# Kernel optimization log

Measured on AMD Instinct MI355X. Metric: run time of the kernel, lower is better.

## Reference

```python
import jax, jax.numpy as jnp
import numpy as np


def _gru_dir(x, Wih, Whh, bih, bhh):
    # x: (B,T,I) -> (B,T,H); torch GRU equations, h0 = 0
    H = Whh.shape[1]
    pre = x @ Wih.T + bih  # (B,T,3H), input projection hoisted out of scan
    def step(h, p):
        gh = h @ Whh.T + bhh
        pr, pz, pn = jnp.split(p, 3, axis=-1)
        gr, gz, gn = jnp.split(gh, 3, axis=-1)
        r = jax.nn.sigmoid(pr + gr)
        z = jax.nn.sigmoid(pz + gz)
        n = jnp.tanh(pn + r * gn)
        h = (1.0 - z) * n + z * h
        return h, h
    h0 = jnp.zeros((x.shape[0], H), x.dtype)
    _, ys = jax.lax.scan(step, h0, jnp.swapaxes(pre, 0, 1))
    return jnp.swapaxes(ys, 0, 1)


def _gru_bidir(x, Wih, Whh, bih, bhh):
    f = _gru_dir(x, Wih[0], Whh[0], bih[0], bhh[0])
    b = _gru_dir(x[:, ::-1], Wih[1], Whh[1], bih[1], bhh[1])[:, ::-1]
    return jnp.concatenate([f, b], axis=-1)


def _forward(inputs, embed, l_Wih, l_Whh, l_bih, l_bhh, r_Wih, r_Whh, r_bih, r_bhh,
             a_Wih, a_Whh, a_bih, a_bhh, Wc1, Wc2, vc, Wb, Wd, vd, Wm, vm, Ws, vs,
             Wp, vp, Wpred):
    x = embed[inputs]  # (B,T,E)
    hl = _gru_bidir(x, l_Wih, l_Whh, l_bih, l_bhh)  # (B,T,2H)
    hr = _gru_bidir(x, r_Wih, r_Whh, r_bih, r_bhh)  # (B,T,2H)
    # co-attention: score[b,i,j] = vc . tanh(Wc1 hl_j + Wc2 hr_i)
    s = jnp.tanh((hl @ Wc1.T)[:, None, :, :] + (hr @ Wc2.T)[:, :, None, :])  # (B,T,T,H)
    ptc = jax.nn.softmax((s @ vc.T)[..., 0], axis=-1) @ hl
    # bilinear: hr (Wb hl)^T
    sjt = jnp.einsum('bid,bjd->bij', hr, hl @ Wb.T)
    ptb = jax.nn.softmax(sjt, axis=-1) @ hl
    # multiplicative: vd . tanh(Wd (hl_j * hr_i))
    p = hl[:, None, :, :] * hr[:, :, None, :]  # (B,T,T,2H)
    ptd = jax.nn.softmax((jnp.tanh(p @ Wd.T) @ vd.T)[..., 0], axis=-1) @ hl
    # subtractive: vm . tanh(Wm (hl_j - hr_i))
    d = hl[:, None, :, :] - hr[:, :, None, :]  # (B,T,T,2H)
    ptm = jax.nn.softmax((jnp.tanh(d @ Wm.T) @ vm.T)[..., 0], axis=-1) @ hl
    # self-attention on hr: vs . tanh(Ws (hr_j * hr_i))
    ss = hr[:, None, :, :] * hr[:, :, None, :]  # (B,T,T,2H)
    pts = jax.nn.softmax((jnp.tanh(ss @ Ws.T) @ vs.T)[..., 0], axis=-1) @ hr
    agg = jnp.concatenate([hr, pts, ptc, ptd, ptb, ptm], axis=-1)  # (B,T,12H)
    ar = _gru_bidir(agg, a_Wih, a_Whh, a_bih, a_bhh)  # (B,T,2H)
    # pooling of hl
    sj = jax.nn.softmax(jnp.swapaxes(jnp.tanh(hl @ Wp.T) @ vp.T, 1, 2), axis=-1)  # (B,1,T)
    rl = sj @ hl  # (B,1,2H)
    # final attention over aggregation
    sj2 = jax.nn.softmax(jnp.swapaxes((ar @ Wc1.T + rl @ Wc2.T) @ vc.T, 1, 2), axis=-1)  # (B,1,T)
    rr = (sj2 @ ar)[:, 0, :]  # (B,2H)
    return jax.nn.sigmoid(rr @ Wpred.T)  # (B,labels)


def setup_inputs() -> dict:
    B, T, V, E, H, L = 4, 256, 30000, 300, 128, 2
    key = jax.random.key(0)
    ks = jax.random.split(key, 40)
    inp = {}
    inp['inputs'] = jax.random.randint(ks[0], (B, T), 0, V)
    inp['embed'] = jax.random.uniform(ks[1], (V, E), jnp.float32, -0.1, 0.1)
    ki = 2
    for name, isz in [('l', E), ('r', E), ('a', 12 * H)]:
        inp[name + '_Wih'] = jax.random.normal(ks[ki], (2, 3 * H, isz), jnp.float32) * 0.05; ki += 1
        inp[name + '_Whh'] = jax.random.normal(ks[ki], (2, 3 * H, H), jnp.float32) * 0.05; ki += 1
        inp[name + '_bih'] = jnp.zeros((2, 3 * H), jnp.float32)
        inp[name + '_bhh'] = jnp.zeros((2, 3 * H), jnp.float32)
    for n, o, i in [('Wc1', H, 2 * H), ('Wc2', H, 2 * H), ('vc', 1, H), ('Wb', 2 * H, 2 * H),
                    ('Wd', H, 2 * H), ('vd', 1, H), ('Wm', H, 2 * H), ('vm', 1, H),
                    ('Ws', H, 2 * H), ('vs', 1, H), ('Wp', H, 2 * H), ('vp', 1, H),
                    ('Wpred', L, 2 * H)]:
        inp[n] = jax.random.normal(ks[ki], (o, i), jnp.float32) * 0.05; ki += 1
    return inp


def reference(inputs, embed, l_Wih, l_Whh, l_bih, l_bhh, r_Wih, r_Whh, r_bih, r_bhh,
              a_Wih, a_Whh, a_bih, a_bhh, Wc1, Wc2, vc, Wb, Wd, vd, Wm, vm, Ws, vs,
              Wp, vp, Wpred):
    return _forward(inputs, embed, l_Wih, l_Whh, l_bih, l_bhh, r_Wih, r_Whh, r_bih,
                    r_bhh, a_Wih, a_Whh, a_bih, a_bhh, Wc1, Wc2, vc, Wb, Wd, vd, Wm,
                    vm, Ws, vs, Wp, vp, Wpred)
```

## Files before the change

### kernel.cpp

```cpp
#include <hip/hip_runtime.h>


#define DEV static __device__ __forceinline__
#define BAR_LGKM() __asm__ volatile("s_waitcnt lgkmcnt(0)\ns_barrier" ::: "memory")

typedef __attribute__((ext_vector_type(4))) float f32x4;
typedef __attribute__((ext_vector_type(8))) short s16x8;
typedef __attribute__((ext_vector_type(4))) unsigned int u32x4;
typedef __attribute__((ext_vector_type(2))) unsigned int u32x2;

constexpr int T = 256, E = 300, EP = 320, H = 128, H2 = 256, H3 = 384, H12 = 1536;
constexpr int M = 1024;
constexpr int STY = 262144;

DEV float b2f(unsigned short h) { return __uint_as_float(((unsigned)h) << 16); }
DEV unsigned short f2b(float f) {
  unsigned u = __float_as_uint(f);
  u += 0x7fff + ((u >> 16) & 1);
  return (unsigned short)(u >> 16);
}
DEV unsigned cvt_pk_bf16(float lo, float hi) {
  unsigned r;
  __asm__("v_cvt_pk_bf16_f32 %0, %1, %2" : "=v"(r) : "v"(lo), "v"(hi));
  return r;
}
DEV float rcp_f(float x) {
  float r;
  __asm__("v_rcp_f32 %0, %1" : "=v"(r) : "v"(x));
  return r;
}
DEV float sigm(float x) { return rcp_f(1.f + __expf(-x)); }
DEV float tanh_f(float x) {
  float e = __expf(2.f * x);
  return __builtin_fmaf(-2.f, rcp_f(e + 1.f), 1.f);
}
DEV float plsel(float x0, float x1) {
  u32x2 r = __builtin_amdgcn_permlane32_swap(
      __float_as_uint(x0), __float_as_uint(x1), false, false);
  return __uint_as_float(r[0]);
}

DEV s16x8 ldfrag(const unsigned short* p) {
  u32x4 v = *(const u32x4*)p;
  return __builtin_bit_cast(s16x8, v);
}
DEV f32x4 mfma16(s16x8 a, s16x8 b, f32x4 c) {
  return __builtin_amdgcn_mfma_f32_16x16x32_bf16(a, b, c, 0, 0, 0);
}


struct StageArgs {
  const float* cs[9]; unsigned short* cd[9]; int cn[9];
  const int* idx; const float* emb; unsigned short* xhi; unsigned short* xlo;
  const float* lW; const float* rW; unsigned short* wpad;
  int bo[12];
};

__global__ void k_stage(StageArgs sa) {
  int blk = blockIdx.x;
  int seg = 0;
  #pragma unroll
  for (int s2 = 1; s2 < 11; ++s2) seg = (blk >= sa.bo[s2]) ? s2 : seg;
  int i = (blk - sa.bo[seg]) * 256 + threadIdx.x;
  if (seg < 9) {
    if (i < sa.cn[seg]) sa.cd[seg][i] = f2b(sa.cs[seg][i]);
    return;
  }
  if (seg == 9) {
    if (i >= M * EP) return;
    int m = i / EP, e = i - m * EP;
    int r = sa.idx[m];
    float v = (e < E) ? sa.emb[(size_t)r * E + e] : 0.f;
    unsigned short hi = f2b(v);
    sa.xhi[i] = hi;
    sa.xlo[i] = f2b(v - b2f(hi));
    return;
  }
  if (i >= 4 * H3 * EP) return;
  int e = i % EP, n = (i / EP) % H3, uu = i / (EP * H3);
  const float* src = (uu < 2 ? sa.lW : sa.rW) + (size_t)((uu & 1) * H3 + n) * E;
  sa.wpad[i] = (e < E) ? f2b(src[e]) : (unsigned short)0;
}


struct GemmDesc {
  const unsigned short* Ahi; const unsigned short* Alo; const unsigned short* W;
  const float* bias; float* Cf; int N; int K; int tr;
};
struct GemmBatch { GemmDesc d[8]; };

DEV void gemm_body(const GemmDesc& g, int mb, int nb, int tid) {
  int lane = tid & 63, w = tid >> 6, quad = lane >> 4, l16 = lane & 15;
  int K = g.K;
  const unsigned short* Ahp = g.Ahi + (size_t)(mb + w * 16 + l16) * K + quad * 8;
  const unsigned short* Alp = g.Alo + (size_t)(mb + w * 16 + l16) * K + quad * 8;
  const unsigned short* Wp = g.W + (size_t)(nb + l16) * K + quad * 8;
  f32x4 acc[4];
  #pragma unroll
  for (int nt = 0; nt < 4; ++nt) acc[nt] = f32x4{0.f, 0.f, 0.f, 0.f};
  for (int k = 0; k < K; k += 32) {
    s16x8 ah = ldfrag(Ahp + k);
    s16x8 al = ldfrag(Alp + k);
    #pragma unroll
    for (int nt = 0; nt < 4; ++nt) {
      s16x8 b = ldfrag(Wp + (size_t)nt * 16 * K + k);
      acc[nt] = mfma16(ah, b, acc[nt]);
      acc[nt] = mfma16(al, b, acc[nt]);
    }
  }
  int mr0 = mb + w * 16 + quad * 4;
  #pragma unroll
  for (int nt = 0; nt < 4; ++nt) {
    int col = nb + nt * 16 + l16;
    float bv = g.bias ? g.bias[col] : 0.f;
    #pragma unroll
    for (int r = 0; r < 4; ++r) {
      if (g.tr)
        g.Cf[(size_t)col * M + (mr0 + r)] = acc[nt][r] + bv;
      else
        g.Cf[(size_t)(mr0 + r) * g.N + col] = acc[nt][r] + bv;
    }
  }
}

__global__ __launch_bounds__(256) void k_gemm(GemmBatch gb) {
  GemmDesc g = gb.d[blockIdx.z];
  int nb = blockIdx.y * 64;
  if (nb >= g.N) return;
  gemm_body(g, blockIdx.x * 64, nb, threadIdx.x);
}


struct RecArgs {
  const unsigned short* whh[4];
  const float* pre[4];
  float* outf[4];
  unsigned short* outhi[4];
  unsigned short* outlo[4];
  unsigned short* agghi[4];
  unsigned short* agglo[4];
  const float* bhh[4];
  int colOff[4];
  int dir[4];
};

#define GRU_STEP(pr_, pz_, pn_, pq_, hcur_, hnxt_)                             \
  {                                                                            \
    float pr = pr_, pz = pz_, pn = pn_;                                        \
    pq_ += pst2;                                                               \
    pr_ = pq_[0] + bh_r; pz_ = pq_[128] + bh_z; pn_ = pq_[256];                \
    const unsigned short* hb_ = hcur_ + l16 * 136 + quad * 8;                  \
    s16x8 ah0 = ldfrag(hb_);                                                   \
    s16x8 ah1 = ldfrag(hb_ + 32);                                              \
    s16x8 ah2 = ldfrag(hb_ + 64);                                              \
    s16x8 ah3 = ldfrag(hb_ + 96);                                              \
    f32x4 z4 = f32x4{0.f, 0.f, 0.f, 0.f};                                      \
    f32x4 aR0 = mfma16(ah0, bq[0][0], z4);                                     \
    f32x4 aR1 = mfma16(ah2, bq[0][2], z4);                                     \
    aR0 = mfma16(ah1, bq[0][1], aR0);                                          \
    aR1 = mfma16(ah3, bq[0][3], aR1);                                          \
    f32x4 aZ0 = mfma16(ah0, bq[1][0], z4);                                     \
    f32x4 aZ1 = mfma16(ah2, bq[1][2], z4);                                     \
    aZ0 = mfma16(ah1, bq[1][1], aZ0);                                          \
    aZ1 = mfma16(ah3, bq[1][3], aZ1);                                          \
    float r0 = (aR0[0] + aR1[0]) + (aR0[1] + aR1[1]);                          \
    float r1v = (aR0[2] + aR1[2]) + (aR0[3] + aR1[3]);                         \
    float rg = sigm(pr + plsel(r0, r1v));                                      \
    f32x4 aN0 = mfma16(ah0, bq[2][0], z4);                                     \
    f32x4 aN1 = mfma16(ah2, bq[2][2], z4);                                     \
    aN0 = mfma16(ah1, bq[2][1], aN0);                                          \
    aN1 = mfma16(ah3, bq[2][3], aN1);                                          \
    float z0 = (aZ0[0] + aZ1[0]) + (aZ0[1] + aZ1[1]);                          \
    float z1 = (aZ0[2] + aZ1[2]) + (aZ0[3] + aZ1[3]);                          \
    float zg = sigm(pz + plsel(z0, z1));                                       \
    float n0 = (aN0[0] + aN1[0]) + (aN0[1] + aN1[1]);                          \
    float n1 = (aN0[2] + aN1[2]) + (aN0[3] + aN1[3]);                          \
    float ng = tanh_f(pn + rg * (plsel(n0, n1) + bh_n));                       \
    hf = __builtin_fmaf(zg, hf - ng, ng);                                      \
    unsigned hp32 = cvt_pk_bf16(hf, hf);                                       \
    float rem = hf - __uint_as_float(hp32 << 16);                              \
    unsigned lp32 = cvt_pk_bf16(rem, rem);                                     \
    unsigned short hi = (unsigned short)hp32;                                  \
    unsigned short lo = (unsigned short)lp32;                                  \
    hnxt_[(2 * b) * 136 + d] = hi;                                             \
    hnxt_[(2 * b + 1) * 136 + d] = lo;                                         \
    *outf_p = hf; *outhi_p = hi; *outlo_p = lo;                                \
    outf_p += ost; outhi_p += ost; outlo_p += ost;                             \
    if (agghi_p) { *agghi_p = hi; *agglo_p = lo; agghi_p += ast; agglo_p += ast; } \
    BAR_LGKM();                                                                \
  }

__global__ __launch_bounds__(512) void k_gru(RecArgs ra) {
  int u = blockIdx.x;
  __shared__ __align__(16) unsigned short hs[2][16 * 136];
  int tid = threadIdx.x, lane = tid & 63, w8 = tid >> 6;
  int quad = lane >> 4, l16 = lane & 15;
  for (int i = tid; i < 2 * 16 * 136; i += 512) ((unsigned short*)hs)[i] = 0;
  const unsigned short* whh = ra.whh[u];
  s16x8 bq[3][4];
  #pragma unroll
  for (int g = 0; g < 3; ++g) {
    int row = g * 128 + w8 * 16 + l16;
    #pragma unroll
    for (int kc = 0; kc < 4; ++kc)
      bq[g][kc] = ldfrag(whh + (size_t)row * H + kc * 32 + quad * 8);
  }
  const float* bhh = ra.bhh[u];
  const float* pre = ra.pre[u];
  int colOff = ra.colOff[u], dir = ra.dir[u];
  int b = ((quad & 1) << 1) | (quad >> 1);
  int d = w8 * 16 + l16;
  float bh_r = bhh[d], bh_z = bhh[d + 128], bh_n = bhh[d + 256];
  float hf = 0.f;
  int t0 = dir ? (T - 1) : 0;
  long pst = dir ? -(long)H3 : (long)H3;
  long pst2 = 2 * pst;
  long ost = dir ? -(long)H2 : (long)H2;
  long ast = dir ? -(long)H12 : (long)H12;
  size_t o0 = (size_t)(b * T + t0) * H2 + colOff + d;
  size_t a0 = (size_t)(b * T + t0) * H12 + colOff + d;
  float* outf_p = ra.outf[u] + o0;
  unsigned short* outhi_p = ra.outhi[u] + o0;
  unsigned short* outlo_p = ra.outlo[u] + o0;
  unsigned short* agghi_p = ra.agghi[u] ? ra.agghi[u] + a0 : nullptr;
  unsigned short* agglo_p = ra.agglo[u] ? ra.agglo[u] + a0 : nullptr;
  const float* pqE = pre + (size_t)(b * T + t0) * H3 + d;
  const float* pqO = pqE + pst;
  float e_pr = pqE[0] + bh_r, e_pz = pqE[128] + bh_z, e_pn = pqE[256];
  float o_pr = pqO[0] + bh_r, o_pz = pqO[128] + bh_z, o_pn = pqO[256];
  __syncthreads();
  for (int s = 0; s < T; s += 2) {
    GRU_STEP(e_pr, e_pz, e_pn, pqE, hs[0], hs[1]);
    GRU_STEP(o_pr, o_pz, o_pn, pqO, hs[1], hs[0]);
  }
}


struct ScMMArgs {
  const unsigned short* Xhi[2];
  const float* Rf; const float* Wt[2]; const float* vt[2];
  float* So[2]; float* So2[2];
};
struct FuseArgs { GemmDesc d[6]; ScMMArgs sm; };

__global__ __launch_bounds__(256, 2) void k_fuse(FuseArgs fa) {
  __shared__ __align__(16) unsigned short w_lds[64 * 256];
  int y = blockIdx.y;
  int tid = threadIdx.x;
  if (y < 6) {
    int xx = blockIdx.x;
    if (xx >= 64) return;
    GemmDesc g = fa.d[y];
    int nb = (xx >> 4) * 64;
    if (nb >= g.N) return;
    gemm_body(g, (xx & 15) * 64, nb, tid);
    return;
  }
  const ScMMArgs& a = fa.sm;
  int which = y - 6;
  int bi = blockIdx.x, b = bi >> 8;
  int type = which >> 1, khb = which & 1;
  const unsigned short* Xhi = a.Xhi[type];
  const float* W = a.Wt[type] + (size_t)khb * 64 * 256;
  const float* v = a.vt[type] + khb * 64;
  float* Sout = khb ? a.So2[type] : a.So[type];
  int lane = tid & 63, w = tid >> 6, quad = lane >> 4, l16 = lane & 15;
  int d4 = tid & 63, rhi = tid >> 6;
  float4 h4 = ((const float4*)(a.Rf + (size_t)bi * 256))[d4];
  #pragma unroll
  for (int it = 0; it < 16; ++it) {
    int kl = it * 4 + rhi;
    float4 w4 = ((const float4*)(W + (size_t)kl * 256))[d4];
    unsigned lo32 = cvt_pk_bf16(w4.x * h4.x, w4.y * h4.y);
    unsigned hi32 = cvt_pk_bf16(w4.z * h4.z, w4.w * h4.w);
    unsigned long long pk = (unsigned long long)lo32 | ((unsigned long long)hi32 << 32);
    int gphys = ((d4 >> 1) + kl) & 31;
    *(unsigned long long*)(w_lds + (size_t)kl * 256 + gphys * 8 + (d4 & 1) * 4) = pk;
  }
  BAR_LGKM();
  f32x4 acc[4][4];
  #pragma unroll
  for (int jj = 0; jj < 4; ++jj)
    #pragma unroll
    for (int c = 0; c < 4; ++c) acc[jj][c] = f32x4{0.f, 0.f, 0.f, 0.f};
  const unsigned short* Xp0 =
      Xhi + (size_t)(b * 256 + w * 4 * 16 + l16) * 256 + quad * 8;
  #pragma unroll 2
  for (int kc = 0; kc < 8; ++kc) {
    s16x8 af[4];
    #pragma unroll
    for (int c = 0; c < 4; ++c) {
      int krow = c * 16 + l16;
      int gp = (kc * 4 + quad + krow) & 31;
      af[c] = ldfrag(w_lds + (size_t)krow * 256 + gp * 8);
    }
    s16x8 bf[4];
    #pragma unroll
    for (int jj = 0; jj < 4; ++jj)
      bf[jj] = ldfrag(Xp0 + (size_t)jj * 16 * 256 + kc * 32);
    #pragma unroll
    for (int jj = 0; jj < 4; ++jj)
      #pragma unroll
      for (int c = 0; c < 4; ++c)
        acc[jj][c] = mfma16(af[c], bf[jj], acc[jj][c]);
  }
  float vv[4][4];
  #pragma unroll
  for (int c = 0; c < 4; ++c)
    #pragma unroll
    for (int r = 0; r < 4; ++r) vv[c][r] = v[c * 16 + quad * 4 + r];
  #pragma unroll
  for (int jj = 0; jj < 4; ++jj) {
    float s = 0.f;
    #pragma unroll
    for (int c = 0; c < 4; ++c)
      #pragma unroll
      for (int r = 0; r < 4; ++r) s += tanh_f(acc[jj][c][r]) * vv[c][r];
    s += __shfl_xor(s, 16);
    s += __shfl_xor(s, 32);
    int jt = w * 4 + jj;
    if (lane < 16) Sout[(size_t)bi * 256 + jt * 16 + l16] = s;
  }
}


struct ScCmbArgs {
  const float *Hc, *Rc, *Hm, *Rm, *HB, *hrf, *vcf, *vmf; float* S;
};

__global__ __launch_bounds__(256, 2) void k_sccmb(ScCmbArgs a) {
  int bi = blockIdx.x;
  int tid = threadIdx.x;
  __shared__ float rc_l[4 * 128];
  __shared__ float rm_l[4 * 128];
  __shared__ float hr_l[4 * 256];
  __shared__ float vc_l[128], vm_l[128];
  int b = bi >> 6, i0 = (bi & 63) << 2;
  int gi0 = b * 256 + i0;
  {
    const float4* hr4 = (const float4*)(a.hrf + (size_t)gi0 * 256);
    ((float4*)hr_l)[tid] = hr4[tid];
    if (tid < 128) {
      const float4* rc4 = (const float4*)(a.Rc + (size_t)gi0 * 128);
      const float4* rm4 = (const float4*)(a.Rm + (size_t)gi0 * 128);
      ((float4*)rc_l)[tid] = rc4[tid];
      ((float4*)rm_l)[tid] = rm4[tid];
      vc_l[tid] = a.vcf[tid]; vm_l[tid] = a.vmf[tid];
    }
  }
  __syncthreads();
  int j = tid;
  size_t cb = (size_t)(b * 256 + j);
  float scq[4], smq[4], sbq[4];
  #pragma unroll
  for (int q = 0; q < 4; ++q) { scq[q] = 0.f; smq[q] = 0.f; sbq[q] = 0.f; }
  for (int k = 0; k < 128; ++k) {
    float hc = a.Hc[(size_t)k * M + cb];
    float hm = a.Hm[(size_t)k * M + cb];
    float vck = vc_l[k], vmk = vm_l[k];
    #pragma unroll
    for (int q = 0; q < 4; ++q) {
      scq[q] += vck * tanh_f(hc + rc_l[q * 128 + k]);
      smq[q] += vmk * tanh_f(hm - rm_l[q * 128 + k]);
    }
  }
  for (int k = 0; k < 256; ++k) {
    float hb = a.HB[(size_t)k * M + cb];
    #pragma unroll
    for (int q = 0; q < 4; ++q) sbq[q] += hb * hr_l[q * 256 + k];
  }
  #pragma unroll
  for (int q = 0; q < 4; ++q) {
    size_t o = (size_t)(gi0 + q) * 256 + j;
    a.S[(size_t)STY * 1 + o] = scq[q];
    a.S[(size_t)STY * 3 + o] = sbq[q];
    a.S[(size_t)STY * 4 + o] = smq[q];
  }
}


__global__ __launch_bounds__(256) void k_wsum(const float* __restrict__ S,
    const float* __restrict__ S2,
    const float* __restrict__ hl_f, const float* __restrict__ hr_f,
    unsigned short* __restrict__ ahi, unsigned short* __restrict__ alo) {
  int it = blockIdx.x, type = blockIdx.y, b = blockIdx.z;
  __shared__ float p_l[8][256];
  __shared__ float red[4];
  int tid = threadIdx.x;
  for (int ii = 0; ii < 8; ++ii) {
    size_t idx = ((size_t)(b * 256 + it * 8 + ii)) * 256 + tid;
    float x = S[(size_t)type * STY + idx];
    if (type == 0) x += S2[idx];
    else if (type == 2) x += S2[(size_t)STY + idx];
    float m = x;
    for (int dl = 32; dl; dl >>= 1) m = fmaxf(m, __shfl_xor(m, dl));
    if ((tid & 63) == 0) red[tid >> 6] = m;
    __syncthreads();
    m = fmaxf(fmaxf(red[0], red[1]), fmaxf(red[2], red[3]));
    __syncthreads();
    float e = __expf(x - m);
    float sum = e;
    for (int dl = 32; dl; dl >>= 1) sum += __shfl_xor(sum, dl);
    if ((tid & 63) == 0) red[tid >> 6] = sum;
    __syncthreads();
    sum = red[0] + red[1] + red[2] + red[3];
    p_l[ii][tid] = e * rcp_f(sum);
    __syncthreads();
  }
  const float* src = (type == 0 ? hr_f : hl_f) + (size_t)b * 256 * 256;
  float acc[8] = {0.f, 0.f, 0.f, 0.f, 0.f, 0.f, 0.f, 0.f};
  for (int j = 0; j < 256; ++j) {
    float hv = src[(size_t)j * 256 + tid];
    #pragma unroll
    for (int ii = 0; ii < 8; ++ii) acc[ii] += p_l[ii][j] * hv;
  }
  int off = 256 * (1 + type);
  #pragma unroll
  for (int ii = 0; ii < 8; ++ii) {
    float vv = acc[ii];
    unsigned short hi = f2b(vv);
    size_t o = (size_t)(b * 256 + it * 8 + ii) * H12 + off + tid;
    ahi[o] = hi;
    alo[o] = f2b(vv - b2f(hi));
  }
}


__global__ __launch_bounds__(256) void k_tail(const float* __restrict__ Hp,
    const float* __restrict__ hl_f, const float* __restrict__ vpf,
    const float* __restrict__ Wc2f, const float* __restrict__ Arc,
    const float* __restrict__ ar_f, const float* __restrict__ vcf,
    const float* __restrict__ Wpredf, float* __restrict__ out) {
  int b = blockIdx.x, tid = threadIdx.x;
  __shared__ float vl[128], wl[256], rvec[256], rlcl[128], red[4];
  if (tid < 128) vl[tid] = vpf[tid];
  __syncthreads();
  const float* hp = Hp + (size_t)(b * 256 + tid) * 128;
  float s = 0.f;
  for (int k = 0; k < 128; ++k) s += vl[k] * tanh_f(hp[k]);
  float m = s;
  for (int dl = 32; dl; dl >>= 1) m = fmaxf(m, __shfl_xor(m, dl));
  if ((tid & 63) == 0) red[tid >> 6] = m;
  __syncthreads();
  m = fmaxf(fmaxf(red[0], red[1]), fmaxf(red[2], red[3]));
  __syncthreads();
  float e = __expf(s - m);
  float sum = e;
  for (int dl = 32; dl; dl >>= 1) sum += __shfl_xor(sum, dl);
  if ((tid & 63) == 0) red[tid >> 6] = sum;
  __syncthreads();
  sum = red[0] + red[1] + red[2] + red[3];
  wl[tid] = e * rcp_f(sum);
  __syncthreads();
  float acc = 0.f;
  for (int t = 0; t < 256; ++t) acc += wl[t] * hl_f[(size_t)(b * 256 + t) * 256 + tid];
  rvec[tid] = acc;
  __syncthreads();
  if (tid < 128) {
    float a2 = 0.f;
    const float* wr = Wc2f + (size_t)tid * 256;
    for (int dk = 0; dk < 256; ++dk) a2 += rvec[dk] * wr[dk];
    rlcl[tid] = a2;
    vl[tid] = vcf[tid];
  }
  __syncthreads();
  const float* ap = Arc + (size_t)(b * 256 + tid) * 128;
  float s2 = 0.f;
  for (int k = 0; k < 128; ++k) s2 += vl[k] * (ap[k] + rlcl[k]);
  m = s2;
  for (int dl = 32; dl; dl >>= 1) m = fmaxf(m, __shfl_xor(m, dl));
  if ((tid & 63) == 0) red[tid >> 6] = m;
  __syncthreads();
  m = fmaxf(fmaxf(red[0], red[1]), fmaxf(red[2], red[3]));
  __syncthreads();
  float e2 = __expf(s2 - m);
  float sum2 = e2;
  for (int dl = 32; dl; dl >>= 1) sum2 += __shfl_xor(sum2, dl);
  if ((tid & 63) == 0) red[tid >> 6] = sum2;
  __syncthreads();
  sum2 = red[0] + red[1] + red[2] + red[3];
  wl[tid] = e2 * rcp_f(sum2);
  __syncthreads();
  float acc2 = 0.f;
  for (int t = 0; t < 256; ++t) acc2 += wl[t] * ar_f[(size_t)(b * 256 + t) * 256 + tid];
  rvec[tid] = acc2;
  __syncthreads();
  if (tid < 2) {
    float o = 0.f;
    const float* wp = Wpredf + (size_t)tid * 256;
    for (int dk = 0; dk < 256; ++dk) o += rvec[dk] * wp[dk];
    out[b * 2 + tid] = sigm(o);
  }
}


extern "C" void kernel_launch(void* const* d_in, const int* in_sizes, int n_in,
                              void* d_out, int out_size, void* d_ws, size_t ws_size,
                              hipStream_t stream) {
  (void)in_sizes; (void)n_in; (void)out_size; (void)ws_size;
  const int* inputs = (const int*)d_in[0];
  const float* embed = (const float*)d_in[1];
  const float* lWih = (const float*)d_in[2];
  const float* lWhh = (const float*)d_in[3];
  const float* lbih = (const float*)d_in[4];
  const float* lbhh = (const float*)d_in[5];
  const float* rWih = (const float*)d_in[6];
  const float* rWhh = (const float*)d_in[7];
  const float* rbih = (const float*)d_in[8];
  const float* rbhh = (const float*)d_in[9];
  const float* aWih = (const float*)d_in[10];
  const float* aWhh = (const float*)d_in[11];
  const float* abih = (const float*)d_in[12];
  const float* abhh = (const float*)d_in[13];
  const float* Wc1 = (const float*)d_in[14];
  const float* Wc2 = (const float*)d_in[15];
  const float* vc  = (const float*)d_in[16];
  const float* Wb  = (const float*)d_in[17];
  const float* Wd  = (const float*)d_in[18];
  const float* vd  = (const float*)d_in[19];
  const float* Wm  = (const float*)d_in[20];
  const float* vmv = (const float*)d_in[21];
  const float* Wsw = (const float*)d_in[22];
  const float* vsv = (const float*)d_in[23];
  const float* Wp  = (const float*)d_in[24];
  const float* vp  = (const float*)d_in[25];
  const float* Wpred = (const float*)d_in[26];

  char* ws = (char*)d_ws;
  size_t off = 0;
  auto alloc = [&](size_t bytes) -> void* {
    void* p = ws + off;
    off += (bytes + 255) & ~(size_t)255;
    return p;
  };
  unsigned short* xhi = (unsigned short*)alloc((size_t)M * EP * 2);
  unsigned short* xlo = (unsigned short*)alloc((size_t)M * EP * 2);
  unsigned short* wpad = (unsigned short*)alloc((size_t)4 * H3 * EP * 2);
  unsigned short* Whh_b = (unsigned short*)alloc((size_t)6 * H3 * H * 2);
  unsigned short* aWih_b = (unsigned short*)alloc((size_t)2 * H3 * H12 * 2);
  unsigned short* Wc1_b = (unsigned short*)alloc((size_t)H * H2 * 2);
  unsigned short* Wc2_b = (unsigned short*)alloc((size_t)H * H2 * 2);
  unsigned short* Wm_b  = (unsigned short*)alloc((size_t)H * H2 * 2);
  unsigned short* Wp_b  = (unsigned short*)alloc((size_t)H * H2 * 2);
  unsigned short* Wb_b  = (unsigned short*)alloc((size_t)H2 * H2 * 2);
  char* region1 = (char*)alloc((size_t)4 * M * H3 * 4);
  float* pre_lr = (float*)region1;
  float* S      = (float*)region1;
  float* pre_a  = (float*)region1;
  float* S2 = (float*)alloc((size_t)2 * STY * 4);
  float* hl_f = (float*)alloc((size_t)M * H2 * 4);
  float* hr_f = (float*)alloc((size_t)M * H2 * 4);
  unsigned short* hl_hi = (unsigned short*)alloc((size_t)M * H2 * 2);
  unsigned short* hl_lo = (unsigned short*)alloc((size_t)M * H2 * 2);
  unsigned short* hr_hi = (unsigned short*)alloc((size_t)M * H2 * 2);
  unsigned short* hr_lo = (unsigned short*)alloc((size_t)M * H2 * 2);
  float* Hc = (float*)alloc((size_t)M * H * 4);
  float* Rc = (float*)alloc((size_t)M * H * 4);
  float* Hm = (float*)alloc((size_t)M * H * 4);
  float* Rm = (float*)alloc((size_t)M * H * 4);
  float* Hp = (float*)alloc((size_t)M * H * 4);
  float* HB = (float*)alloc((size_t)M * H2 * 4);
  unsigned short* agg_hi = (unsigned short*)alloc((size_t)M * H12 * 2);
  unsigned short* agg_lo = (unsigned short*)alloc((size_t)M * H12 * 2);
  float* ar_f = (float*)alloc((size_t)M * H2 * 4);
  unsigned short* ar_hi = (unsigned short*)alloc((size_t)M * H2 * 2);
  unsigned short* ar_lo = (unsigned short*)alloc((size_t)M * H2 * 2);
  float* Arc = (float*)alloc((size_t)M * H * 4);

  StageArgs sa{};
  sa.cs[0] = lWhh;  sa.cd[0] = Whh_b;                 sa.cn[0] = 2 * H3 * H;
  sa.cs[1] = rWhh;  sa.cd[1] = Whh_b + 2 * H3 * H;    sa.cn[1] = 2 * H3 * H;
  sa.cs[2] = aWhh;  sa.cd[2] = Whh_b + 4 * H3 * H;    sa.cn[2] = 2 * H3 * H;
  sa.cs[3] = aWih;  sa.cd[3] = aWih_b;                sa.cn[3] = 2 * H3 * H12;
  sa.cs[4] = Wc1;   sa.cd[4] = Wc1_b;                 sa.cn[4] = H * H2;
  sa.cs[5] = Wc2;   sa.cd[5] = Wc2_b;                 sa.cn[5] = H * H2;
  sa.cs[6] = Wm;    sa.cd[6] = Wm_b;                  sa.cn[6] = H * H2;
  sa.cs[7] = Wp;    sa.cd[7] = Wp_b;                  sa.cn[7] = H * H2;
  sa.cs[8] = Wb;    sa.cd[8] = Wb_b;                  sa.cn[8] = H2 * H2;
  sa.idx = inputs; sa.emb = embed; sa.xhi = xhi; sa.xlo = xlo;
  sa.lW = lWih; sa.rW = rWih; sa.wpad = wpad;
  {
    int acc0 = 0;
    sa.bo[0] = 0;
    for (int s = 0; s < 9; ++s) { acc0 += (sa.cn[s] + 255) / 256; sa.bo[s + 1] = acc0; }
    acc0 += (M * EP + 255) / 256;       sa.bo[10] = acc0;
    acc0 += (4 * H3 * EP + 255) / 256;  sa.bo[11] = acc0;
  }
  k_stage<<<dim3(sa.bo[11]), dim3(256), 0, stream>>>(sa);

  GemmBatch ga{};
  const float* biases[4] = { lbih, lbih + H3, rbih, rbih + H3 };
  for (int u = 0; u < 4; ++u)
    ga.d[u] = GemmDesc{ xhi, xlo, wpad + (size_t)u * H3 * EP, biases[u],
                        pre_lr + (size_t)u * M * H3, H3, EP, 0 };
  k_gemm<<<dim3(16, 6, 4), dim3(256), 0, stream>>>(ga);

  RecArgs r1{};
  r1.whh[0] = Whh_b;               r1.whh[1] = Whh_b + H3 * H;
  r1.whh[2] = Whh_b + 2 * H3 * H;  r1.whh[3] = Whh_b + 3 * H3 * H;
  for (int u = 0; u < 4; ++u) r1.pre[u] = pre_lr + (size_t)u * M * H3;
  r1.outf[0] = r1.outf[1] = hl_f; r1.outf[2] = r1.outf[3] = hr_f;
  r1.outhi[0] = r1.outhi[1] = hl_hi; r1.outhi[2] = r1.outhi[3] = hr_hi;
  r1.outlo[0] = r1.outlo[1] = hl_lo; r1.outlo[2] = r1.outlo[3] = hr_lo;
  r1.agghi[0] = r1.agghi[1] = nullptr; r1.agghi[2] = r1.agghi[3] = agg_hi;
  r1.agglo[0] = r1.agglo[1] = nullptr; r1.agglo[2] = r1.agglo[3] = agg_lo;
  r1.bhh[0] = lbhh; r1.bhh[1] = lbhh + H3; r1.bhh[2] = rbhh; r1.bhh[3] = rbhh + H3;
  r1.colOff[0] = 0; r1.colOff[1] = H; r1.colOff[2] = 0; r1.colOff[3] = H;
  r1.dir[0] = 0; r1.dir[1] = 1; r1.dir[2] = 0; r1.dir[3] = 1;
  k_gru<<<dim3(4), dim3(512), 0, stream>>>(r1);

  FuseArgs fu{};
  fu.d[0] = GemmDesc{ hl_hi, hl_lo, Wc1_b, nullptr, Hc, H, H2, 1 };
  fu.d[1] = GemmDesc{ hr_hi, hr_lo, Wc2_b, nullptr, Rc, H, H2, 0 };
  fu.d[2] = GemmDesc{ hl_hi, hl_lo, Wm_b, nullptr, Hm, H, H2, 1 };
  fu.d[3] = GemmDesc{ hr_hi, hr_lo, Wm_b, nullptr, Rm, H, H2, 0 };
  fu.d[4] = GemmDesc{ hl_hi, hl_lo, Wb_b, nullptr, HB, H2, H2, 1 };
  fu.d[5] = GemmDesc{ hl_hi, hl_lo, Wp_b, nullptr, Hp, H, H2, 0 };
  fu.sm.Xhi[0] = hl_hi; fu.sm.Wt[0] = Wd;  fu.sm.vt[0] = vd;
  fu.sm.So[0] = S + (size_t)2 * STY;
  fu.sm.Xhi[1] = hr_hi; fu.sm.Wt[1] = Wsw; fu.sm.vt[1] = vsv;
  fu.sm.So[1] = S + (size_t)0 * STY;
  fu.sm.So2[0] = S2 + (size_t)STY;
  fu.sm.So2[1] = S2;
  fu.sm.Rf = hr_f;
  k_fuse<<<dim3(M, 10), dim3(256), 0, stream>>>(fu);

  ScCmbArgs scb{};
  scb.Hc = Hc; scb.Rc = Rc; scb.Hm = Hm; scb.Rm = Rm; scb.HB = HB;
  scb.hrf = hr_f; scb.vcf = vc; scb.vmf = vmv; scb.S = S;
  k_sccmb<<<dim3(256), dim3(256), 0, stream>>>(scb);

  k_wsum<<<dim3(32, 5, 4), dim3(256), 0, stream>>>(S, S2, hl_f, hr_f, agg_hi, agg_lo);

  GemmBatch gc{};
  gc.d[0] = GemmDesc{ agg_hi, agg_lo, aWih_b, abih, pre_a, H3, H12, 0 };
  gc.d[1] = GemmDesc{ agg_hi, agg_lo, aWih_b + (size_t)H3 * H12, abih + H3,
                      pre_a + (size_t)M * H3, H3, H12, 0 };
  k_gemm<<<dim3(16, 6, 2), dim3(256), 0, stream>>>(gc);

  RecArgs r2{};
  r2.whh[0] = Whh_b + 4 * H3 * H; r2.whh[1] = Whh_b + 5 * H3 * H;
  r2.whh[2] = r2.whh[3] = Whh_b + 4 * H3 * H;
  r2.pre[0] = pre_a; r2.pre[1] = pre_a + (size_t)M * H3;
  r2.pre[2] = r2.pre[3] = pre_a;
  r2.outf[0] = r2.outf[1] = r2.outf[2] = r2.outf[3] = ar_f;
  r2.outhi[0] = r2.outhi[1] = r2.outhi[2] = r2.outhi[3] = ar_hi;
  r2.outlo[0] = r2.outlo[1] = r2.outlo[2] = r2.outlo[3] = ar_lo;
  for (int u = 0; u < 4; ++u) { r2.agghi[u] = nullptr; r2.agglo[u] = nullptr; }
  r2.bhh[0] = abhh; r2.bhh[1] = abhh + H3; r2.bhh[2] = r2.bhh[3] = abhh;
  r2.colOff[0] = 0; r2.colOff[1] = H; r2.colOff[2] = r2.colOff[3] = 0;
  r2.dir[0] = 0; r2.dir[1] = 1; r2.dir[2] = r2.dir[3] = 0;
  k_gru<<<dim3(2), dim3(512), 0, stream>>>(r2);

  GemmBatch gd{};
  gd.d[0] = GemmDesc{ ar_hi, ar_lo, Wc1_b, nullptr, Arc, H, H2, 0 };
  k_gemm<<<dim3(16, 2, 1), dim3(256), 0, stream>>>(gd);

  k_tail<<<dim3(4), dim3(256), 0, stream>>>(Hp, hl_f, vp, Wc2, Arc, ar_f, vc, Wpred,
                                            (float*)d_out);
}
```

Baseline: 676.0 us.

## Merge split-K score blocks into single 512-thread block per row

The multiplicative and self-attention score kernel previously split the 128-wide hidden dimension across two 256-thread blocks, writing partial scores to a second buffer that the softmax kernel then summed. It now uses one 512-thread block per row that stages all 128 weight rows in LDS and computes the full reduction directly, removing the S2 buffer and its extra reads and writes. Each wave now holds 2x8 accumulator tiles and reuses each B fragment across eight MFMAs. The fused GEMM branch is adapted so each 512-thread block covers two 64-row tiles. The cost is doubled LDS per block and heavier register use, which may reduce occupancy.

```diff
diff --git a/kernel.cpp b/kernel.cpp
--- a/kernel.cpp
+++ b/kernel.cpp
@@ -239,37 +239,37 @@
 struct ScMMArgs {
   const unsigned short* Xhi[2];
   const float* Rf; const float* Wt[2]; const float* vt[2];
-  float* So[2]; float* So2[2];
+  float* So[2];
 };
 struct FuseArgs { GemmDesc d[6]; ScMMArgs sm; };
 
-__global__ __launch_bounds__(256, 2) void k_fuse(FuseArgs fa) {
-  __shared__ __align__(16) unsigned short w_lds[64 * 256];
+__global__ __launch_bounds__(512, 2) void k_fuse(FuseArgs fa) {
+  __shared__ __align__(16) unsigned short w_lds[128 * 256];
   int y = blockIdx.y;
   int tid = threadIdx.x;
   if (y < 6) {
     int xx = blockIdx.x;
-    if (xx >= 64) return;
+    if (xx >= 32) return;
     GemmDesc g = fa.d[y];
-    int nb = (xx >> 4) * 64;
+    int nb = (xx >> 3) * 64;
     if (nb >= g.N) return;
-    gemm_body(g, (xx & 15) * 64, nb, tid);
+    int mb = (xx & 7) * 128 + (tid >> 8) * 64;
+    gemm_body(g, mb, nb, tid & 255);
     return;
   }
   const ScMMArgs& a = fa.sm;
-  int which = y - 6;
+  int type = y - 6;
   int bi = blockIdx.x, b = bi >> 8;
-  int type = which >> 1, khb = which & 1;
   const unsigned short* Xhi = a.Xhi[type];
-  const float* W = a.Wt[type] + (size_t)khb * 64 * 256;
-  const float* v = a.vt[type] + khb * 64;
-  float* Sout = khb ? a.So2[type] : a.So[type];
+  const float* W = a.Wt[type];
+  const float* v = a.vt[type];
+  float* Sout = a.So[type];
   int lane = tid & 63, w = tid >> 6, quad = lane >> 4, l16 = lane & 15;
   int d4 = tid & 63, rhi = tid >> 6;
   float4 h4 = ((const float4*)(a.Rf + (size_t)bi * 256))[d4];
   #pragma unroll
   for (int it = 0; it < 16; ++it) {
-    int kl = it * 4 + rhi;
+    int kl = it * 8 + rhi;
     float4 w4 = ((const float4*)(W + (size_t)kl * 256))[d4];
     unsigned lo32 = cvt_pk_bf16(w4.x * h4.x, w4.y * h4.y);
     unsigned hi32 = cvt_pk_bf16(w4.z * h4.z, w4.w * h4.w);
@@ -278,47 +278,37 @@
     *(unsigned long long*)(w_lds + (size_t)kl * 256 + gphys * 8 + (d4 & 1) * 4) = pk;
   }
   BAR_LGKM();
-  f32x4 acc[4][4];
-  #pragma unroll
-  for (int jj = 0; jj < 4; ++jj)
-    #pragma unroll
-    for (int c = 0; c < 4; ++c) acc[jj][c] = f32x4{0.f, 0.f, 0.f, 0.f};
+  f32x4 acc[2][8];
+  #pragma unroll
+  for (int jj = 0; jj < 2; ++jj)
+    #pragma unroll
+    for (int c = 0; c < 8; ++c) acc[jj][c] = f32x4{0.f, 0.f, 0.f, 0.f};
   const unsigned short* Xp0 =
-      Xhi + (size_t)(b * 256 + w * 4 * 16 + l16) * 256 + quad * 8;
+      Xhi + (size_t)(b * 256 + w * 2 * 16 + l16) * 256 + quad * 8;
   #pragma unroll 2
   for (int kc = 0; kc < 8; ++kc) {
-    s16x8 af[4];
-    #pragma unroll
-    for (int c = 0; c < 4; ++c) {
+    s16x8 bf0 = ldfrag(Xp0 + kc * 32);
+    s16x8 bf1 = ldfrag(Xp0 + (size_t)16 * 256 + kc * 32);
+    #pragma unroll
+    for (int c = 0; c < 8; ++c) {
       int krow = c * 16 + l16;
       int gp = (kc * 4 + quad + krow) & 31;
-      af[c] = ldfrag(w_lds + (size_t)krow * 256 + gp * 8);
+      s16x8 af = ldfrag(w_lds + (size_t)krow * 256 + gp * 8);
+      acc[0][c] = mfma16(af, bf0, acc[0][c]);
+      acc[1][c] = mfma16(af, bf1, acc[1][c]);
     }
-    s16x8 bf[4];
-    #pragma unroll
-    for (int jj = 0; jj < 4; ++jj)
-      bf[jj] = ldfrag(Xp0 + (size_t)jj * 16 * 256 + kc * 32);
-    #pragma unroll
-    for (int jj = 0; jj < 4; ++jj)
+  }
+  #pragma unroll
+  for (int jj = 0; jj < 2; ++jj) {
+    float s = 0.f;
+    #pragma unroll
+    for (int c = 0; c < 8; ++c)
       #pragma unroll
-      for (int c = 0; c < 4; ++c)
-        acc[jj][c] = mfma16(af[c], bf[jj], acc[jj][c]);
-  }
-  float vv[4][4];
-  #pragma unroll
-  for (int c = 0; c < 4; ++c)
-    #pragma unroll
-    for (int r = 0; r < 4; ++r) vv[c][r] = v[c * 16 + quad * 4 + r];
-  #pragma unroll
-  for (int jj = 0; jj < 4; ++jj) {
-    float s = 0.f;
-    #pragma unroll
-    for (int c = 0; c < 4; ++c)
-      #pragma unroll
-      for (int r = 0; r < 4; ++r) s += tanh_f(acc[jj][c][r]) * vv[c][r];
+      for (int r = 0; r < 4; ++r)
+        s += tanh_f(acc[jj][c][r]) * v[c * 16 + quad * 4 + r];
     s += __shfl_xor(s, 16);
     s += __shfl_xor(s, 32);
-    int jt = w * 4 + jj;
+    int jt = w * 2 + jj;
     if (lane < 16) Sout[(size_t)bi * 256 + jt * 16 + l16] = s;
   }
 }
@@ -380,7 +370,6 @@
 
 
 __global__ __launch_bounds__(256) void k_wsum(const float* __restrict__ S,
-    const float* __restrict__ S2,
     const float* __restrict__ hl_f, const float* __restrict__ hr_f,
     unsigned short* __restrict__ ahi, unsigned short* __restrict__ alo) {
   int it = blockIdx.x, type = blockIdx.y, b = blockIdx.z;
@@ -390,8 +379,6 @@
   for (int ii = 0; ii < 8; ++ii) {
     size_t idx = ((size_t)(b * 256 + it * 8 + ii)) * 256 + tid;
     float x = S[(size_t)type * STY + idx];
-    if (type == 0) x += S2[idx];
-    else if (type == 2) x += S2[(size_t)STY + idx];
     float m = x;
     for (int dl = 32; dl; dl >>= 1) m = fmaxf(m, __shfl_xor(m, dl));
     if ((tid & 63) == 0) red[tid >> 6] = m;
@@ -547,7 +534,6 @@
   float* pre_lr = (float*)region1;
   float* S      = (float*)region1;
   float* pre_a  = (float*)region1;
-  float* S2 = (float*)alloc((size_t)2 * STY * 4);
   float* hl_f = (float*)alloc((size_t)M * H2 * 4);
   float* hr_f = (float*)alloc((size_t)M * H2 * 4);
   unsigned short* hl_hi = (unsigned short*)alloc((size_t)M * H2 * 2);
@@ -620,17 +606,15 @@
   fu.sm.So[0] = S + (size_t)2 * STY;
   fu.sm.Xhi[1] = hr_hi; fu.sm.Wt[1] = Wsw; fu.sm.vt[1] = vsv;
   fu.sm.So[1] = S + (size_t)0 * STY;
-  fu.sm.So2[0] = S2 + (size_t)STY;
-  fu.sm.So2[1] = S2;
   fu.sm.Rf = hr_f;
-  k_fuse<<<dim3(M, 10), dim3(256), 0, stream>>>(fu);
+  k_fuse<<<dim3(M, 8), dim3(512), 0, stream>>>(fu);
 
   ScCmbArgs scb{};
   scb.Hc = Hc; scb.Rc = Rc; scb.Hm = Hm; scb.Rm = Rm; scb.HB = HB;
   scb.hrf = hr_f; scb.vcf = vc; scb.vmf = vmv; scb.S = S;
   k_sccmb<<<dim3(256), dim3(256), 0, stream>>>(scb);
 
-  k_wsum<<<dim3(32, 5, 4), dim3(256), 0, stream>>>(S, S2, hl_f, hr_f, agg_hi, agg_lo);
+  k_wsum<<<dim3(32, 5, 4), dim3(256), 0, stream>>>(S, hl_f, hr_f, agg_hi, agg_lo);
 
   GemmBatch gc{};
   gc.d[0] = GemmDesc{ agg_hi, agg_lo, aWih_b, abih, pre_a, H3, H12, 0 };
```

Result: faster. 658.8 us (-2.5%).
